# Kernel optimization log

Hardware: AMD Instinct MI355X
Metric: run time of the kernel (lower is better)

Reference implementation:

```python
import jax, jax.numpy as jnp
import numpy as np

NUM_STEPS = 10  # module __init__ default


def setup_inputs() -> dict:
    key = jax.random.key(0)
    k1, k2, k3 = jax.random.split(key, 3)
    B, D = 256, 64
    outputs = jax.random.normal(k1, (B, D), dtype=jnp.float32)
    targets = jax.random.normal(k2, (B, D), dtype=jnp.float32)
    # Christoffel symbols, scaled small so the RK2 integration stays well-behaved
    gamma = jax.random.normal(k3, (B, D, D, D), dtype=jnp.float32) * 0.1
    return {"outputs": outputs, "targets": targets, "christoffel_symbols": gamma}


def _accel(gamma, v):
    # a_i = - Gamma^i_{jk} v^j v^k  (vectorized form of the quadruple loop)
    return -jnp.einsum('bijk,bj,bk->bi', gamma, v, v)


def _geodesic_loss(x0, x1, gamma):
    dt = 1.0 / NUM_STEPS
    v = (x1 - x0) / NUM_STEPS
    v = v / (jnp.linalg.norm(v, axis=1, keepdims=True) + 1e-8)

    def step(carry, _):
        traj, vel = carry
        a = _accel(gamma, vel)
        mid_vel = vel + 0.5 * a * dt
        mid_a = _accel(gamma, mid_vel)
        vel = vel + mid_a * dt
        traj = traj + vel * dt
        return (traj, vel), traj

    (traj, _), path = jax.lax.scan(step, (x0, v), None, length=NUM_STEPS)
    full_path = jnp.concatenate([x0[None], path], axis=0)  # [S+1, B, D]

    target_penalty = jnp.mean(jnp.linalg.norm(traj - x1, axis=1))
    # second differences for interior points i = 1..S-1
    second = full_path[2:] - 2.0 * full_path[1:-1] + full_path[:-2]  # [S-1, B, D]
    smoothness = jnp.sum(jnp.mean(jnp.linalg.norm(second, axis=-1), axis=-1))
    return target_penalty + 0.1 * smoothness


def reference(outputs, targets, christoffel_symbols):
    gamma = christoffel_symbols
    euclid = jnp.mean(jnp.linalg.norm(outputs - targets, axis=1))
    geo = _geodesic_loss(outputs, targets, gamma)
    # torch code returns plain L2 mean when all Christoffel symbols are zero
    return jnp.where(jnp.all(gamma == 0), euclid, geo)
```

## Files before the change

### kernel.cpp

```cpp
#include <hip/hip_runtime.h>


#define NSTEPS 10
#define BATCH 256
#define DIM 64
#define TPB 1024
#define ROWLEN 4096
#define NPACK 2080
#define WS_ACC_FLOATS 64

__device__ __forceinline__ float waveSum(float v) {
    #pragma unroll
    for (int off = 32; off; off >>= 1) v += __shfl_xor(v, off, 64);
    return v;
}

__global__ void init_ws_kernel(unsigned* ws) {
    if (threadIdx.x < 4) ws[threadIdx.x] = 0u;
}

__global__ __launch_bounds__(TPB, 1)
void geo_main_kernel(const float* __restrict__ x0g,
                     const float* __restrict__ x1g,
                     const float* __restrict__ gam,
                     float* __restrict__ ws,
                     float* __restrict__ pack,
                     int use_pack)
{
    __shared__ float vel[DIM];
    __shared__ float mvel[DIM];
    __shared__ float acc[DIM];
    __shared__ float wp[ROWLEN];
    __shared__ uchar2 lut[NPACK];
    __shared__ float rowbuf[2][ROWLEN];

    const int b    = blockIdx.x;
    const int t    = threadIdx.x;
    const int wave = t >> 6;
    const int lane = t & 63;
    const float dt = 1.0f / NSTEPS;

    for (int e = t; e < ROWLEN; e += TPB) {
        int j = e >> 6, k = e & 63;
        if (k >= j) {
            int idx = j * DIM - (j * (j - 1)) / 2 + (k - j);
            lut[idx] = make_uchar2((unsigned char)j, (unsigned char)k);
        }
    }

    float x1r = 0.f, fpPrev = 0.f, fpCur = 0.f, trajr = 0.f;
    if (wave == 0) {
        float x0r = x0g[b * DIM + lane];
        x1r       = x1g[b * DIM + lane];
        float d0  = x1r - x0r;
        float nrm = sqrtf(waveSum(d0 * d0));
        if (lane == 0) atomicAdd(&ws[1], nrm * (1.0f / BATCH));
        float v  = d0 * dt;
        float nv = nrm * dt;
        v = v / (nv + 1e-8f);
        vel[lane] = v;
        trajr  = x0r;
        fpCur  = x0r;
    }
    __syncthreads();

    unsigned nzflag = 0;

    if (use_pack) {
        const float4* g4 = (const float4*)(gam + (size_t)b * DIM * ROWLEN);
        float4 pre = g4[t];
        for (int i = 0; i < DIM; ++i) {
            ((float4*)rowbuf[i & 1])[t] = pre;
            nzflag |= (pre.x != 0.f) | (pre.y != 0.f) | (pre.z != 0.f) | (pre.w != 0.f);
            __syncthreads();
            if (i + 1 < DIM) pre = g4[(size_t)(i + 1) * (ROWLEN / 4) + t];
            const float* rb = rowbuf[i & 1];
            float* prow = pack + ((size_t)b * DIM + i) * NPACK;
            #pragma unroll
            for (int rep = 0; rep < 3; ++rep) {
                int e = t + rep * TPB;
                if (e < NPACK) {
                    uchar2 jk = lut[e];
                    float vsym = rb[jk.x * DIM + jk.y];
                    if (jk.x != jk.y) vsym += rb[jk.y * DIM + jk.x];
                    prow[e] = vsym;
                }
            }
            __syncthreads();
        }
    }

    const float* mat = use_pack ? pack + (size_t)b * DIM * NPACK
                                : gam  + (size_t)b * DIM * ROWLEN;
    const int L = use_pack ? NPACK : ROWLEN;

    auto accel = [&](const float* vsrc, bool doflag) {
        __syncthreads();
        for (int e = t; e < L; e += TPB) {
            int j, k;
            if (use_pack) { uchar2 jk = lut[e]; j = jk.x; k = jk.y; }
            else          { j = e >> 6; k = e & 63; }
            wp[e] = vsrc[j] * vsrc[k];
        }
        __syncthreads();
        const int full = L >> 6;
        #pragma unroll
        for (int rr = 0; rr < 4; ++rr) {
            const int i = wave * 4 + rr;
            const float* mrow = mat + (size_t)i * L;
            float s = 0.f;
            for (int u = 0; u < full; ++u) {
                float g = mrow[lane + (u << 6)];
                if (doflag) nzflag |= (g != 0.f);
                s += g * wp[lane + (u << 6)];
            }
            int rem = lane + (full << 6);
            if (rem < L) {
                float g = mrow[rem];
                if (doflag) nzflag |= (g != 0.f);
                s += g * wp[rem];
            }
            s = waveSum(s);
            if (lane == 0) acc[i] = -s;
        }
        __syncthreads();
    };

    float smooth = 0.f;
    for (int s = 0; s < NSTEPS; ++s) {
        accel(vel, (!use_pack) && (s == 0));
        if (wave == 0) mvel[lane] = vel[lane] + 0.5f * dt * acc[lane];
        accel(mvel, false);
        if (wave == 0) {
            float vnew = vel[lane] + dt * acc[lane];
            vel[lane]  = vnew;
            float fpNext = trajr + dt * vnew;
            trajr = fpNext;
            if (s >= 1) {
                float sec = fpNext - 2.f * fpCur + fpPrev;
                smooth += sqrtf(waveSum(sec * sec));
            }
            fpPrev = fpCur;
            fpCur  = fpNext;
        }
    }

    unsigned long long bal = __ballot(nzflag != 0);
    if (lane == 0 && bal) atomicOr((unsigned*)ws + 2, 1u);

    if (wave == 0) {
        float dl  = trajr - x1r;
        float tgt = sqrtf(waveSum(dl * dl));
        if (lane == 0) atomicAdd(&ws[0], (tgt + 0.1f * smooth) * (1.0f / BATCH));
    }
}

__global__ void finalize_kernel(const float* ws, float* out) {
    unsigned flag = ((const unsigned*)ws)[2];
    out[0] = flag ? ws[0] : ws[1];
}

extern "C" void kernel_launch(void* const* d_in, const int* in_sizes, int n_in,
                              void* d_out, int out_size, void* d_ws, size_t ws_size,
                              hipStream_t stream) {
    const float* x0  = (const float*)d_in[0];
    const float* x1  = (const float*)d_in[1];
    const float* gam = (const float*)d_in[2];
    float* ws   = (float*)d_ws;
    float* pack = (float*)((char*)d_ws + WS_ACC_FLOATS * sizeof(float));

    const size_t need = WS_ACC_FLOATS * sizeof(float)
                      + (size_t)BATCH * DIM * NPACK * sizeof(float);
    const int use_pack = (ws_size >= need) ? 1 : 0;

    init_ws_kernel<<<1, 64, 0, stream>>>((unsigned*)ws);
    geo_main_kernel<<<BATCH, TPB, 0, stream>>>(x0, x1, gam, ws, pack, use_pack);
    finalize_kernel<<<1, 1, 0, stream>>>(ws, (float*)d_out);
}
```

Measured before the change: 755.9 us.

## Template kernel on packing mode, vectorize packed matvec, pad transpose buffer

Turns the runtime use_pack switch into a template parameter so each variant gets its own shared-memory sizing and no runtime branches. The packed accel path now loads matrix rows as float4 with all loads issued up front and processes two rows at a time. The row buffer used in the symmetrization pass is padded to stride 65 to avoid LDS bank conflicts on the transposed reads. The cost is higher register use from holding 16 float4 loads per thread.

```diff
diff --git a/kernel.cpp b/kernel.cpp
--- a/kernel.cpp
+++ b/kernel.cpp
@@ -7,6 +7,7 @@
 #define TPB 1024
 #define ROWLEN 4096
 #define NPACK 2080
+#define RBSTRIDE 65
 #define WS_ACC_FLOATS 64
 
 __device__ __forceinline__ float waveSum(float v) {
@@ -19,20 +20,20 @@
     if (threadIdx.x < 4) ws[threadIdx.x] = 0u;
 }
 
+template<int PACKED>
 __global__ __launch_bounds__(TPB, 1)
 void geo_main_kernel(const float* __restrict__ x0g,
                      const float* __restrict__ x1g,
                      const float* __restrict__ gam,
                      float* __restrict__ ws,
-                     float* __restrict__ pack,
-                     int use_pack)
+                     float* __restrict__ pack)
 {
     __shared__ float vel[DIM];
     __shared__ float mvel[DIM];
     __shared__ float acc[DIM];
-    __shared__ float wp[ROWLEN];
-    __shared__ uchar2 lut[NPACK];
-    __shared__ float rowbuf[2][ROWLEN];
+    __shared__ float wp[PACKED ? NPACK : ROWLEN];
+    __shared__ uchar2 lut[PACKED ? NPACK : 1];
+    __shared__ float rowbuf[PACKED ? 2 * DIM * RBSTRIDE : 1];
 
     const int b    = blockIdx.x;
     const int t    = threadIdx.x;
@@ -40,11 +41,13 @@
     const int lane = t & 63;
     const float dt = 1.0f / NSTEPS;
 
-    for (int e = t; e < ROWLEN; e += TPB) {
-        int j = e >> 6, k = e & 63;
-        if (k >= j) {
-            int idx = j * DIM - (j * (j - 1)) / 2 + (k - j);
-            lut[idx] = make_uchar2((unsigned char)j, (unsigned char)k);
+    if constexpr (PACKED) {
+        for (int e = t; e < ROWLEN; e += TPB) {
+            int j = e >> 6, k = e & 63;
+            if (k >= j) {
+                int idx = j * DIM - (j * (j - 1)) / 2 + (k - j);
+                lut[idx] = make_uchar2((unsigned char)j, (unsigned char)k);
+            }
         }
     }
 
@@ -66,23 +69,27 @@
 
     unsigned nzflag = 0;
 
-    if (use_pack) {
+    if constexpr (PACKED) {
         const float4* g4 = (const float4*)(gam + (size_t)b * DIM * ROWLEN);
         float4 pre = g4[t];
         for (int i = 0; i < DIM; ++i) {
-            ((float4*)rowbuf[i & 1])[t] = pre;
-            nzflag |= (pre.x != 0.f) | (pre.y != 0.f) | (pre.z != 0.f) | (pre.w != 0.f);
+            {
+                float* rb = &rowbuf[(i & 1) * DIM * RBSTRIDE];
+                float* dst = rb + (t >> 4) * RBSTRIDE + ((t & 15) << 2);
+                dst[0] = pre.x; dst[1] = pre.y; dst[2] = pre.z; dst[3] = pre.w;
+                nzflag |= (pre.x != 0.f) | (pre.y != 0.f) | (pre.z != 0.f) | (pre.w != 0.f);
+            }
             __syncthreads();
             if (i + 1 < DIM) pre = g4[(size_t)(i + 1) * (ROWLEN / 4) + t];
-            const float* rb = rowbuf[i & 1];
+            const float* rb = &rowbuf[(i & 1) * DIM * RBSTRIDE];
             float* prow = pack + ((size_t)b * DIM + i) * NPACK;
             #pragma unroll
             for (int rep = 0; rep < 3; ++rep) {
                 int e = t + rep * TPB;
                 if (e < NPACK) {
                     uchar2 jk = lut[e];
-                    float vsym = rb[jk.x * DIM + jk.y];
-                    if (jk.x != jk.y) vsym += rb[jk.y * DIM + jk.x];
+                    float vsym = rb[jk.x * RBSTRIDE + jk.y];
+                    if (jk.x != jk.y) vsym += rb[jk.y * RBSTRIDE + jk.x];
                     prow[e] = vsym;
                 }
             }
@@ -90,36 +97,74 @@
         }
     }
 
-    const float* mat = use_pack ? pack + (size_t)b * DIM * NPACK
-                                : gam  + (size_t)b * DIM * ROWLEN;
-    const int L = use_pack ? NPACK : ROWLEN;
-
-    auto accel = [&](const float* vsrc, bool doflag) {
-        __syncthreads();
-        for (int e = t; e < L; e += TPB) {
-            int j, k;
-            if (use_pack) { uchar2 jk = lut[e]; j = jk.x; k = jk.y; }
-            else          { j = e >> 6; k = e & 63; }
-            wp[e] = vsrc[j] * vsrc[k];
-        }
-        __syncthreads();
-        const int full = L >> 6;
+    const float* mat = PACKED ? pack + (size_t)b * DIM * NPACK
+                              : gam  + (size_t)b * DIM * ROWLEN;
+
+    auto accel_packed = [&](const float* vsrc) {
+        __syncthreads();
+        #pragma unroll
+        for (int rep = 0; rep < 3; ++rep) {
+            int e = t + rep * TPB;
+            if (e < NPACK) {
+                uchar2 jk = lut[e];
+                wp[e] = vsrc[jk.x] * vsrc[jk.y];
+            }
+        }
+        __syncthreads();
+        const float4* wp4 = (const float4*)wp;
+        const bool tl = lane < 8;
+        #pragma unroll
+        for (int p = 0; p < 2; ++p) {
+            const int i0 = (wave << 2) + (p << 1);
+            const int i1 = i0 + 1;
+            const float4* r0 = (const float4*)(mat + (size_t)i0 * NPACK);
+            const float4* r1 = (const float4*)(mat + (size_t)i1 * NPACK);
+            float4 g0[8], g1[8];
+            #pragma unroll
+            for (int u = 0; u < 8; ++u) g0[u] = r0[lane + (u << 6)];
+            #pragma unroll
+            for (int u = 0; u < 8; ++u) g1[u] = r1[lane + (u << 6)];
+            float4 gt0 = make_float4(0.f, 0.f, 0.f, 0.f);
+            float4 gt1 = gt0;
+            if (tl) { gt0 = r0[512 + lane]; gt1 = r1[512 + lane]; }
+            float s0 = 0.f, s1 = 0.f;
+            #pragma unroll
+            for (int u = 0; u < 8; ++u) {
+                float4 w = wp4[lane + (u << 6)];
+                s0 += g0[u].x * w.x; s1 += g1[u].x * w.x;
+                s0 += g0[u].y * w.y; s1 += g1[u].y * w.y;
+                s0 += g0[u].z * w.z; s1 += g1[u].z * w.z;
+                s0 += g0[u].w * w.w; s1 += g1[u].w * w.w;
+            }
+            if (tl) {
+                float4 w = wp4[512 + lane];
+                s0 += gt0.x * w.x + gt0.y * w.y + gt0.z * w.z + gt0.w * w.w;
+                s1 += gt1.x * w.x + gt1.y * w.y + gt1.z * w.z + gt1.w * w.w;
+            }
+            s0 = waveSum(s0); s1 = waveSum(s1);
+            if (lane == 0) { acc[i0] = -s0; acc[i1] = -s1; }
+        }
+        __syncthreads();
+    };
+
+    auto accel_raw = [&](const float* vsrc, bool doflag) {
+        __syncthreads();
+        #pragma unroll
+        for (int rep = 0; rep < 4; ++rep) {
+            int e = t + rep * TPB;
+            wp[e] = vsrc[e >> 6] * vsrc[e & 63];
+        }
+        __syncthreads();
         #pragma unroll
         for (int rr = 0; rr < 4; ++rr) {
-            const int i = wave * 4 + rr;
-            const float* mrow = mat + (size_t)i * L;
+            const int i = (wave << 2) + rr;
+            const float* mrow = mat + (size_t)i * ROWLEN;
             float s = 0.f;
-            for (int u = 0; u < full; ++u) {
+            for (int u = 0; u < 64; ++u) {
                 float g = mrow[lane + (u << 6)];
                 if (doflag) nzflag |= (g != 0.f);
                 s += g * wp[lane + (u << 6)];
             }
-            int rem = lane + (full << 6);
-            if (rem < L) {
-                float g = mrow[rem];
-                if (doflag) nzflag |= (g != 0.f);
-                s += g * wp[rem];
-            }
             s = waveSum(s);
             if (lane == 0) acc[i] = -s;
         }
@@ -128,9 +173,11 @@
 
     float smooth = 0.f;
     for (int s = 0; s < NSTEPS; ++s) {
-        accel(vel, (!use_pack) && (s == 0));
+        if constexpr (PACKED) accel_packed(vel);
+        else                  accel_raw(vel, s == 0);
         if (wave == 0) mvel[lane] = vel[lane] + 0.5f * dt * acc[lane];
-        accel(mvel, false);
+        if constexpr (PACKED) accel_packed(mvel);
+        else                  accel_raw(mvel, false);
         if (wave == 0) {
             float vnew = vel[lane] + dt * acc[lane];
             vel[lane]  = vnew;
@@ -174,6 +221,9 @@
     const int use_pack = (ws_size >= need) ? 1 : 0;
 
     init_ws_kernel<<<1, 64, 0, stream>>>((unsigned*)ws);
-    geo_main_kernel<<<BATCH, TPB, 0, stream>>>(x0, x1, gam, ws, pack, use_pack);
+    if (use_pack)
+        geo_main_kernel<1><<<BATCH, TPB, 0, stream>>>(x0, x1, gam, ws, pack);
+    else
+        geo_main_kernel<0><<<BATCH, TPB, 0, stream>>>(x0, x1, gam, ws, pack);
     finalize_kernel<<<1, 1, 0, stream>>>(ws, (float*)d_out);
 }
```

After: 968.9 us. +28.2%, slower.

## Keep symmetrized Christoffel rows in registers instead of a global pack buffer

Applied to the files above, without the earlier changes.

Each block now symmetrizes its gamma slice two rows at a time through padded shared memory. Each wave then holds its four packed rows in registers (float4 chunks) for all RK2 steps. This removes the global pack scratch buffer, its write and its twenty re-reads per block, and replaces the LUT with per-thread computed (j,k) pairs. It costs heavy register pressure (144 VGPRs for the matrix rows at 1024 threads), which risks spills, and it adds extra barriers in the step loop.

```diff
diff --git a/kernel.cpp b/kernel.cpp
--- a/kernel.cpp
+++ b/kernel.cpp
@@ -5,13 +5,27 @@
 #define BATCH 256
 #define DIM 64
 #define TPB 1024
-#define ROWLEN 4096
+#define RBS 65
+#define RBF (DIM * RBS)
 #define NPACK 2080
-#define WS_ACC_FLOATS 64
+#define NPADF 2304
+#define NCH 9
 
 __device__ __forceinline__ float waveSum(float v) {
     #pragma unroll
     for (int off = 32; off; off >>= 1) v += __shfl_xor(v, off, 64);
+    return v;
+}
+
+__device__ __forceinline__ void unpack_e(int e, int& j, int& k) {
+    int jj = 0;
+    while (e >= DIM - jj) { e -= DIM - jj; ++jj; }
+    j = jj; k = jj + e;
+}
+
+__device__ __forceinline__ float symf(const float* rb, int j, int k) {
+    float v = rb[j * RBS + k];
+    if (j != k) v += rb[k * RBS + j];
     return v;
 }
 
@@ -23,16 +37,11 @@
 void geo_main_kernel(const float* __restrict__ x0g,
                      const float* __restrict__ x1g,
                      const float* __restrict__ gam,
-                     float* __restrict__ ws,
-                     float* __restrict__ pack,
-                     int use_pack)
+                     float* __restrict__ ws)
 {
-    __shared__ float vel[DIM];
-    __shared__ float mvel[DIM];
-    __shared__ float acc[DIM];
-    __shared__ float wp[ROWLEN];
-    __shared__ uchar2 lut[NPACK];
-    __shared__ float rowbuf[2][ROWLEN];
+    __shared__ float rowbuf[2 * RBF];
+    __shared__ float pkbuf[2 * NPADF];
+    __shared__ float vel[DIM], mvel[DIM], acc[DIM];
 
     const int b    = blockIdx.x;
     const int t    = threadIdx.x;
@@ -40,13 +49,10 @@
     const int lane = t & 63;
     const float dt = 1.0f / NSTEPS;
 
-    for (int e = t; e < ROWLEN; e += TPB) {
-        int j = e >> 6, k = e & 63;
-        if (k >= j) {
-            int idx = j * DIM - (j * (j - 1)) / 2 + (k - j);
-            lut[idx] = make_uchar2((unsigned char)j, (unsigned char)k);
-        }
-    }
+    int j0, k0, j1, k1, j2 = 0, k2 = 0;
+    unpack_e(t,        j0, k0);
+    unpack_e(t + 1024, j1, k1);
+    if (t < 32) unpack_e(t + 2048, j2, k2);
 
     float x1r = 0.f, fpPrev = 0.f, fpCur = 0.f, trajr = 0.f;
     if (wave == 0) {
@@ -57,80 +63,93 @@
         if (lane == 0) atomicAdd(&ws[1], nrm * (1.0f / BATCH));
         float v  = d0 * dt;
         float nv = nrm * dt;
-        v = v / (nv + 1e-8f);
-        vel[lane] = v;
-        trajr  = x0r;
-        fpCur  = x0r;
+        vel[lane] = v / (nv + 1e-8f);
+        trajr = x0r;
+        fpCur = x0r;
+    }
+
+    float4 gm[4][NCH];
+    unsigned nzflag = 0;
+    const float4* g4 = (const float4*)(gam + (size_t)b * DIM * DIM * DIM);
+
+    float4 pre0 = g4[t];
+    float4 pre1 = g4[1024 + t];
+    #pragma unroll
+    for (int ip = 0; ip < 32; ++ip) {
+        {
+            float* d0p = rowbuf +       (t >> 4) * RBS + ((t & 15) << 2);
+            float* d1p = rowbuf + RBF + (t >> 4) * RBS + ((t & 15) << 2);
+            d0p[0] = pre0.x; d0p[1] = pre0.y; d0p[2] = pre0.z; d0p[3] = pre0.w;
+            d1p[0] = pre1.x; d1p[1] = pre1.y; d1p[2] = pre1.z; d1p[3] = pre1.w;
+            nzflag |= (pre0.x != 0.f) | (pre0.y != 0.f) | (pre0.z != 0.f) | (pre0.w != 0.f)
+                    | (pre1.x != 0.f) | (pre1.y != 0.f) | (pre1.z != 0.f) | (pre1.w != 0.f);
+        }
+        __syncthreads();
+        if (ip + 1 < 32) {
+            pre0 = g4[(size_t)(2 * ip + 2) * 1024 + t];
+            pre1 = g4[(size_t)(2 * ip + 3) * 1024 + t];
+        }
+        {
+            const float* rb0 = rowbuf;
+            const float* rb1 = rowbuf + RBF;
+            float* pk0 = pkbuf;
+            float* pk1 = pkbuf + NPADF;
+            pk0[t]        = symf(rb0, j0, k0);
+            pk1[t]        = symf(rb1, j0, k0);
+            pk0[t + 1024] = symf(rb0, j1, k1);
+            pk1[t + 1024] = symf(rb1, j1, k1);
+            if (t < 32) {
+                pk0[t + 2048] = symf(rb0, j2, k2);
+                pk1[t + 2048] = symf(rb1, j2, k2);
+            } else if (t < 256) {
+                pk0[t + 2048] = 0.f;
+                pk1[t + 2048] = 0.f;
+            }
+        }
+        __syncthreads();
+        if (wave == (ip >> 1)) {
+            const float4* pk40 = (const float4*)pkbuf;
+            const float4* pk41 = (const float4*)(pkbuf + NPADF);
+            const int r0 = (ip & 1) * 2;
+            #pragma unroll
+            for (int u = 0; u < NCH; ++u) gm[r0][u]     = pk40[lane + (u << 6)];
+            #pragma unroll
+            for (int u = 0; u < NCH; ++u) gm[r0 + 1][u] = pk41[lane + (u << 6)];
+        }
     }
     __syncthreads();
 
-    unsigned nzflag = 0;
-
-    if (use_pack) {
-        const float4* g4 = (const float4*)(gam + (size_t)b * DIM * ROWLEN);
-        float4 pre = g4[t];
-        for (int i = 0; i < DIM; ++i) {
-            ((float4*)rowbuf[i & 1])[t] = pre;
-            nzflag |= (pre.x != 0.f) | (pre.y != 0.f) | (pre.z != 0.f) | (pre.w != 0.f);
-            __syncthreads();
-            if (i + 1 < DIM) pre = g4[(size_t)(i + 1) * (ROWLEN / 4) + t];
-            const float* rb = rowbuf[i & 1];
-            float* prow = pack + ((size_t)b * DIM + i) * NPACK;
-            #pragma unroll
-            for (int rep = 0; rep < 3; ++rep) {
-                int e = t + rep * TPB;
-                if (e < NPACK) {
-                    uchar2 jk = lut[e];
-                    float vsym = rb[jk.x * DIM + jk.y];
-                    if (jk.x != jk.y) vsym += rb[jk.y * DIM + jk.x];
-                    prow[e] = vsym;
-                }
-            }
-            __syncthreads();
+    float* wp = pkbuf;
+    auto accel = [&](const float* vsrc) {
+        wp[t]        = vsrc[j0] * vsrc[k0];
+        wp[t + 1024] = vsrc[j1] * vsrc[k1];
+        if (t < 32)       wp[t + 2048] = vsrc[j2] * vsrc[k2];
+        else if (t < 256) wp[t + 2048] = 0.f;
+        __syncthreads();
+        const float4* wp4 = (const float4*)wp;
+        float s0 = 0.f, s1 = 0.f, s2 = 0.f, s3 = 0.f;
+        #pragma unroll
+        for (int u = 0; u < NCH; ++u) {
+            float4 w = wp4[lane + (u << 6)];
+            s0 += gm[0][u].x * w.x + gm[0][u].y * w.y + gm[0][u].z * w.z + gm[0][u].w * w.w;
+            s1 += gm[1][u].x * w.x + gm[1][u].y * w.y + gm[1][u].z * w.z + gm[1][u].w * w.w;
+            s2 += gm[2][u].x * w.x + gm[2][u].y * w.y + gm[2][u].z * w.z + gm[2][u].w * w.w;
+            s3 += gm[3][u].x * w.x + gm[3][u].y * w.y + gm[3][u].z * w.z + gm[3][u].w * w.w;
         }
-    }
-
-    const float* mat = use_pack ? pack + (size_t)b * DIM * NPACK
-                                : gam  + (size_t)b * DIM * ROWLEN;
-    const int L = use_pack ? NPACK : ROWLEN;
-
-    auto accel = [&](const float* vsrc, bool doflag) {
-        __syncthreads();
-        for (int e = t; e < L; e += TPB) {
-            int j, k;
-            if (use_pack) { uchar2 jk = lut[e]; j = jk.x; k = jk.y; }
-            else          { j = e >> 6; k = e & 63; }
-            wp[e] = vsrc[j] * vsrc[k];
-        }
-        __syncthreads();
-        const int full = L >> 6;
-        #pragma unroll
-        for (int rr = 0; rr < 4; ++rr) {
-            const int i = wave * 4 + rr;
-            const float* mrow = mat + (size_t)i * L;
-            float s = 0.f;
-            for (int u = 0; u < full; ++u) {
-                float g = mrow[lane + (u << 6)];
-                if (doflag) nzflag |= (g != 0.f);
-                s += g * wp[lane + (u << 6)];
-            }
-            int rem = lane + (full << 6);
-            if (rem < L) {
-                float g = mrow[rem];
-                if (doflag) nzflag |= (g != 0.f);
-                s += g * wp[rem];
-            }
-            s = waveSum(s);
-            if (lane == 0) acc[i] = -s;
+        s0 = waveSum(s0); s1 = waveSum(s1); s2 = waveSum(s2); s3 = waveSum(s3);
+        if (lane == 0) {
+            const int i0 = wave << 2;
+            acc[i0] = -s0; acc[i0 + 1] = -s1; acc[i0 + 2] = -s2; acc[i0 + 3] = -s3;
         }
         __syncthreads();
     };
 
     float smooth = 0.f;
     for (int s = 0; s < NSTEPS; ++s) {
-        accel(vel, (!use_pack) && (s == 0));
+        accel(vel);
         if (wave == 0) mvel[lane] = vel[lane] + 0.5f * dt * acc[lane];
-        accel(mvel, false);
+        __syncthreads();
+        accel(mvel);
         if (wave == 0) {
             float vnew = vel[lane] + dt * acc[lane];
             vel[lane]  = vnew;
@@ -143,6 +162,7 @@
             fpPrev = fpCur;
             fpCur  = fpNext;
         }
+        __syncthreads();
     }
 
     unsigned long long bal = __ballot(nzflag != 0);
@@ -166,14 +186,9 @@
     const float* x0  = (const float*)d_in[0];
     const float* x1  = (const float*)d_in[1];
     const float* gam = (const float*)d_in[2];
-    float* ws   = (float*)d_ws;
-    float* pack = (float*)((char*)d_ws + WS_ACC_FLOATS * sizeof(float));
-
-    const size_t need = WS_ACC_FLOATS * sizeof(float)
-                      + (size_t)BATCH * DIM * NPACK * sizeof(float);
-    const int use_pack = (ws_size >= need) ? 1 : 0;
+    float* ws = (float*)d_ws;
 
     init_ws_kernel<<<1, 64, 0, stream>>>((unsigned*)ws);
-    geo_main_kernel<<<BATCH, TPB, 0, stream>>>(x0, x1, gam, ws, pack, use_pack);
+    geo_main_kernel<<<BATCH, TPB, 0, stream>>>(x0, x1, gam, ws);
     finalize_kernel<<<1, 1, 0, stream>>>(ws, (float*)d_out);
 }
```

New measurement: 1.003 ms. 32.7% more time.
